# Kernel tuning notes

Measured on AMD Instinct MI355X. Metric: run time of the kernel, lower is better.

The kernel has to match this reference:

```python
import jax, jax.numpy as jnp
import numpy as np

EPS = 1e-12


def _sq_dists(x, y):
    # x: [B, N1, 3], y: [B, N2, 3] -> squared pairwise distances [B, N1, N2]
    x2 = jnp.sum(x * x, axis=-1)            # [B, N1]
    y2 = jnp.sum(y * y, axis=-1)            # [B, N2]
    xy = jnp.einsum('bnd,bmd->bnm', x, y)   # [B, N1, N2]
    d = x2[:, :, None] + y2[:, None, :] - 2.0 * xy
    return jnp.maximum(d, 0.0)


def setup_inputs() -> dict:
    key = jax.random.key(0)
    k1, k2 = jax.random.split(key)
    xyz1 = jax.random.normal(k1, (8, 8192, 3), dtype=jnp.float32)
    xyz2 = jax.random.normal(k2, (8, 8192, 3), dtype=jnp.float32)
    return {"xyz1": xyz1, "xyz2": xyz2}


def reference(xyz1, xyz2):
    d = _sq_dists(xyz1, xyz2)                       # [B, N1, N2]
    dist1 = jnp.min(d, axis=2)                      # nearest in xyz2 for each xyz1 point
    dist2 = jnp.min(d, axis=1)                      # nearest in xyz1 for each xyz2 point
    dist1 = jnp.sqrt(jnp.maximum(dist1, EPS))
    dist2 = jnp.sqrt(jnp.maximum(dist2, EPS))
    per_batch = (jnp.mean(dist1, axis=1) + jnp.mean(dist2, axis=1)) / 2.0  # [B]
    return jnp.mean(per_batch)
```

## Files before the change

### kernel.cpp

```cpp
#include <hip/hip_runtime.h>
#include <math.h>


#define NPTS   8192
#define NB     8
#define NPC    (NB * NPTS)
#define BLOCK  256
#define CHUNK  1024
#define COLS   NPTS
#define TOTALQ (2 * NPC)
#define EPSV   1e-12f
#define FXSCALE 67108864.0

typedef _Float16 v8h  __attribute__((ext_vector_type(8)));
typedef float    v16f __attribute__((ext_vector_type(16)));

__global__ __launch_bounds__(256) void chamfer_prep(
    const float* __restrict__ xyz1, const float* __restrict__ xyz2,
    v8h* __restrict__ form, unsigned long long* __restrict__ counter)
{
    const int gid = blockIdx.x * 256 + threadIdx.x;
    if (gid == 0) counter[0] = 0ULL;
    const float* __restrict__ src = (gid < NPC) ? xyz1 : xyz2;
    const int i = (gid < NPC) ? gid : gid - NPC;
    float x = src[3 * i], y = src[3 * i + 1], z = src[3 * i + 2];
    _Float16 xh = (_Float16)x, yh = (_Float16)y, zh = (_Float16)z;
    float xf = (float)xh, yf = (float)yh, zf = (float)zh;
    float n = fmaf(xf, xf, fmaf(yf, yf, zf * zf));
    v8h bv = {};
    bv[0] = xh; bv[1] = yh; bv[2] = zh;
    bv[3] = (_Float16)n; bv[4] = (_Float16)1.0f;
    form[gid] = bv;
}

#define MFMA(va, vb) __builtin_amdgcn_mfma_f32_32x32x16_f16((va), (vb), vzero, 0, 0, 0)

__device__ __forceinline__ unsigned umin2(unsigned a, unsigned b) {
    return a < b ? a : b;
}

__global__ __launch_bounds__(BLOCK, 4) void chamfer_mfma_min(
    const v8h* __restrict__ form, unsigned long long* __restrict__ counter)
{
    const int bid = blockIdx.x;
    const int rb  = bid & 31;
    const int b   = (bid >> 5) & 7;
    const int dir = (bid >> 8) & 1;

    const v8h* __restrict__ qf = form + (size_t)dir * NPC + (size_t)b * NPTS;
    const v8h* __restrict__ tf = form + (size_t)(1 - dir) * NPC + (size_t)b * NPTS;

    const int tid  = threadIdx.x;
    const int lane = tid & 63;
    const int w    = tid >> 6;
    const int c31  = lane & 31;
    const int rowbase = rb * 256;

    v8h a0 = {}, a1 = {};
    if (lane < 32) {
        const _Float16 m2 = (_Float16)(-2.0f);
        v8h f = qf[rowbase + w * 64 + lane];
        a0[0] = m2 * f[0]; a0[1] = m2 * f[1]; a0[2] = m2 * f[2];
        a0[3] = (_Float16)1.0f; a0[4] = f[3];
        f = qf[rowbase + w * 64 + 32 + lane];
        a1[0] = m2 * f[0]; a1[1] = m2 * f[1]; a1[2] = m2 * f[2];
        a1[3] = (_Float16)1.0f; a1[4] = f[3];
    }

    unsigned rm0[16], rm1[16];
#pragma unroll
    for (int r = 0; r < 16; ++r) { rm0[r] = 0x7F7F7F7FU; rm1[r] = 0x7F7F7F7FU; }

    __shared__ v8h bsh[CHUNK];
    const v16f vzero = {};

    for (int ch = 0; ch < COLS / CHUNK; ++ch) {
        __syncthreads();
        const v8h* __restrict__ g = tf + ch * CHUNK;
#pragma unroll
        for (int k = 0; k < CHUNK / BLOCK; ++k)
            bsh[k * BLOCK + tid] = g[k * BLOCK + tid];
        __syncthreads();

#pragma unroll
        for (int cc = 0; cc < CHUNK / 64; ++cc) {
            const v8h b0 = bsh[cc * 64 + c31];
            const v8h b1 = bsh[cc * 64 + 32 + c31];
            __builtin_amdgcn_s_setprio(1);
            v16f p0 = MFMA(a0, b0);
            v16f q0 = MFMA(a0, b1);
            v16f p1 = MFMA(a1, b0);
            v16f q1 = MFMA(a1, b1);
            __builtin_amdgcn_s_setprio(0);
#pragma unroll
            for (int r = 0; r < 16; ++r)
                rm0[r] = umin2(rm0[r], umin2(__builtin_bit_cast(unsigned, p0[r]),
                                             __builtin_bit_cast(unsigned, q0[r])));
#pragma unroll
            for (int r = 0; r < 16; ++r)
                rm1[r] = umin2(rm1[r], umin2(__builtin_bit_cast(unsigned, p1[r]),
                                             __builtin_bit_cast(unsigned, q1[r])));
        }
    }

    float acc = 0.0f;
#pragma unroll
    for (int s = 0; s < 2; ++s) {
#pragma unroll
        for (int r = 0; r < 16; ++r) {
            unsigned u = s ? rm1[r] : rm0[r];
            u = umin2(u, __shfl_xor(u, 1));
            u = umin2(u, __shfl_xor(u, 2));
            u = umin2(u, __shfl_xor(u, 4));
            u = umin2(u, __shfl_xor(u, 8));
            u = umin2(u, __shfl_xor(u, 16));
            if ((lane & 31) == 0) {
                float v = __builtin_bit_cast(float, u);
                acc += sqrtf(fmaxf(fmaxf(v, 0.0f), EPSV));
            }
        }
    }
    acc += __shfl_xor(acc, 32);

    __syncthreads();
    float* red = (float*)bsh;
    if (lane == 0) red[w] = acc;
    __syncthreads();
    if (tid == 0) {
        float s = red[0] + red[1] + red[2] + red[3];
        unsigned long long fx = (unsigned long long)((double)s * FXSCALE + 0.5);
        atomicAdd(counter, fx);
    }
}

__global__ void chamfer_finalize(
    const unsigned long long* __restrict__ counter, float* __restrict__ out)
{
    out[0] = (float)((double)counter[0] * (1.0 / FXSCALE) / (double)TOTALQ);
}

extern "C" void kernel_launch(void* const* d_in, const int* in_sizes, int n_in,
                              void* d_out, int out_size, void* d_ws, size_t ws_size,
                              hipStream_t stream) {
    const float* xyz1 = (const float*)d_in[0];
    const float* xyz2 = (const float*)d_in[1];
    float* out = (float*)d_out;

    v8h* formbuf = (v8h*)d_ws;
    unsigned long long* counter = (unsigned long long*)(formbuf + TOTALQ);

    chamfer_prep<<<TOTALQ / 256, 256, 0, stream>>>(xyz1, xyz2, formbuf, counter);
    chamfer_mfma_min<<<2 * NB * 32, BLOCK, 0, stream>>>(formbuf, counter);
    chamfer_finalize<<<1, 1, 0, stream>>>(counter, out);
}
```

Before: 45.57 us.

## Double-buffer target chunks in LDS with async global_load_lds prefetch

Replaces the synchronous global-to-register-to-LDS copy of each target chunk with a two-slot LDS buffer filled by direct global_load_lds, prefetching the next chunk while MFMAs run on the current one. This cuts the barriers per chunk from two to one and hides global load latency behind compute. It also removes the s_setprio hints around the MFMA group. LDS use doubles to 32 KB per block, which could limit occupancy at four blocks per CU.

```diff
diff --git a/kernel.cpp b/kernel.cpp
--- a/kernel.cpp
+++ b/kernel.cpp
@@ -7,7 +7,7 @@
 #define NPC    (NB * NPTS)
 #define BLOCK  256
 #define CHUNK  1024
-#define COLS   NPTS
+#define NCH    (NPTS / CHUNK)
 #define TOTALQ (2 * NPC)
 #define EPSV   1e-12f
 #define FXSCALE 67108864.0
@@ -56,6 +56,21 @@
     const int c31  = lane & 31;
     const int rowbase = rb * 256;
 
+    __shared__ v8h bsh[2][CHUNK];
+
+#define STAGE(nb, ch)                                                        \
+    {                                                                        \
+        const v8h* gsrc = tf + (ch) * CHUNK;                                 \
+        _Pragma("unroll")                                                    \
+        for (int k = 0; k < CHUNK / BLOCK; ++k)                              \
+            __builtin_amdgcn_global_load_lds(                                \
+                (const __attribute__((address_space(1))) unsigned*)          \
+                    (gsrc + k * BLOCK + tid),                                \
+                (__attribute__((address_space(3))) unsigned*)                \
+                    (&bsh[nb][k * BLOCK + tid]),                             \
+                16, 0, 0);                                                   \
+    }
+
     v8h a0 = {}, a1 = {};
     if (lane < 32) {
         const _Float16 m2 = (_Float16)(-2.0f);
@@ -71,27 +86,24 @@
 #pragma unroll
     for (int r = 0; r < 16; ++r) { rm0[r] = 0x7F7F7F7FU; rm1[r] = 0x7F7F7F7FU; }
 
-    __shared__ v8h bsh[CHUNK];
     const v16f vzero = {};
 
-    for (int ch = 0; ch < COLS / CHUNK; ++ch) {
-        __syncthreads();
-        const v8h* __restrict__ g = tf + ch * CHUNK;
-#pragma unroll
-        for (int k = 0; k < CHUNK / BLOCK; ++k)
-            bsh[k * BLOCK + tid] = g[k * BLOCK + tid];
-        __syncthreads();
+    STAGE(0, 0);
+    asm volatile("s_waitcnt vmcnt(0)" ::: "memory");
+    __syncthreads();
+
+    for (int ch = 0; ch < NCH; ++ch) {
+        const int cur = ch & 1;
+        if (ch + 1 < NCH) STAGE(cur ^ 1, ch + 1);
 
 #pragma unroll
         for (int cc = 0; cc < CHUNK / 64; ++cc) {
-            const v8h b0 = bsh[cc * 64 + c31];
-            const v8h b1 = bsh[cc * 64 + 32 + c31];
-            __builtin_amdgcn_s_setprio(1);
+            const v8h b0 = bsh[cur][cc * 64 + c31];
+            const v8h b1 = bsh[cur][cc * 64 + 32 + c31];
             v16f p0 = MFMA(a0, b0);
             v16f q0 = MFMA(a0, b1);
             v16f p1 = MFMA(a1, b0);
             v16f q1 = MFMA(a1, b1);
-            __builtin_amdgcn_s_setprio(0);
 #pragma unroll
             for (int r = 0; r < 16; ++r)
                 rm0[r] = umin2(rm0[r], umin2(__builtin_bit_cast(unsigned, p0[r]),
@@ -101,6 +113,9 @@
                 rm1[r] = umin2(rm1[r], umin2(__builtin_bit_cast(unsigned, p1[r]),
                                              __builtin_bit_cast(unsigned, q1[r])));
         }
+
+        asm volatile("s_waitcnt vmcnt(0)" ::: "memory");
+        __syncthreads();
     }
 
     float acc = 0.0f;
```

New measurement: 55.63 us. 1.22x slower.
